# Kernel optimization log

Hardware: AMD Instinct MI355X
Metric: run time of the kernel (lower is better)

Reference implementation:

```python
import jax, jax.numpy as jnp
import numpy as np

D = 1024  # d = D_in // 3
GAMMA = 5.0
EPS_NORM = 1e-5
EPS_W = 1e-8


def batch_affine_norm(x, g, b):
    # normalize over batch+time dims, per-feature affine
    mean = x.mean(axis=(0, 1))
    var = x.var(axis=(0, 1))
    return (x - mean) / jnp.sqrt(var + EPS_NORM) * g + b


def block(xi, w, b, a, g, beta):
    # xi: (B,T,d) -> (B,T,d,3)
    # PositiveLinearHK(1->3): softplus-positive weight + bias, per channel
    h = xi[..., None] * jax.nn.softplus(w) + b          # (B,T,d,3)
    # SingleStiefelProjector(3): orthogonalize learned 3x3 via QR, apply
    Q, _ = jnp.linalg.qr(a)                             # (d,3,3)
    h = jnp.einsum('btdi,dij->btdj', h, Q)
    return batch_affine_norm(h, g, beta)


def setup_inputs() -> dict:
    key = jax.random.key(0)
    ks = jax.random.split(key, 20)
    B, T = 4, 2048
    inp = {'x': jax.random.normal(ks[0], (B, T, 3 * D), dtype=jnp.float32)}
    i = 1
    for p in ('q', 'k', 'v'):
        inp['w' + p] = jax.random.normal(ks[i], (D, 3), dtype=jnp.float32) * 0.5; i += 1
        inp['b' + p] = jnp.zeros((D, 3), dtype=jnp.float32)
        inp['a' + p] = jax.random.normal(ks[i], (D, 3, 3), dtype=jnp.float32); i += 1
        inp['g' + p] = jnp.ones((D, 3), dtype=jnp.float32)
        inp['beta' + p] = jnp.zeros((D, 3), dtype=jnp.float32)
    inp['g_out'] = jnp.ones((D,), dtype=jnp.float32)
    inp['b_out'] = jnp.zeros((D,), dtype=jnp.float32)
    return inp


def reference(x, wq, bq, aq, gq, betaq, wk, bk, ak, gk, betak, wv, bv, av, gv, betav, g_out, b_out):
    d = D
    Qp = block(x[..., :d], wq, bq, aq, gq, betaq)        # (B,T,d,3)
    Kp = block(x[..., d:2 * d], wk, bk, ak, gk, betak)
    Vp = block(x[..., 2 * d:], wv, bv, av, gv, betav)
    scores = jax.nn.sigmoid(GAMMA * (Qp * Kp))
    weights = scores / (scores.sum(axis=-1, keepdims=True) + EPS_W)
    out = (weights * Vp).sum(axis=-1)                    # (B,T,d)
    return batch_affine_norm(out, g_out, b_out)
```

## Files before the change

### kernel.cpp

```cpp
#include <hip/hip_runtime.h>
#include <math.h>

namespace {

constexpr int DD = 1024;
constexpr int NC = 3072;
constexpr int NG = 768;
constexpr int DG = 256;
constexpr int NROWS = 8192;
constexpr int CH1 = 64;
constexpr int CH2 = 256;
constexpr float GAMMA = 5.0f;
constexpr float EPS_NORM = 1e-5f;
constexpr float EPS_W = 1e-8f;
constexpr float ZCLAMP = 15.0f;

struct Params {
  const float *x;
  const float *wq, *aq, *gq, *betaq;
  const float *wk, *ak, *gk, *betak;
  const float *wv, *av, *gv, *betav;
  const float *g_out, *b_out;
  float *out;
  float *psum, *psq;
  float *A_arr, *B_arr;
  float *opsum, *opsq;
  float *om, *osc, *ob;
  float *o_arr;
};

__device__ __forceinline__ void acc4(float4& s, float4& q, float4 v) {
  s.x += v.x; s.y += v.y; s.z += v.z; s.w += v.w;
  q.x += v.x * v.x; q.y += v.y * v.y; q.z += v.z * v.z; q.w += v.w * v.w;
}
__device__ __forceinline__ void add4(float4& s, float4 v) {
  s.x += v.x; s.y += v.y; s.z += v.z; s.w += v.w;
}

__device__ __forceinline__ void qr_coef(const Params& P, int c, float mean, float var) {
  int p = c >> 10;
  int d = c & (DD - 1);
  const float* w    = (p == 0) ? P.wq    : (p == 1) ? P.wk    : P.wv;
  const float* a    = (p == 0) ? P.aq    : (p == 1) ? P.ak    : P.av;
  const float* g    = (p == 0) ? P.gq    : (p == 1) ? P.gk    : P.gv;
  const float* beta = (p == 0) ? P.betaq : (p == 1) ? P.betak : P.betav;
  float gam = (p == 0) ? GAMMA : 1.0f;

  float A[3][3];
  #pragma unroll
  for (int i = 0; i < 3; ++i)
    #pragma unroll
    for (int j = 0; j < 3; ++j) A[i][j] = a[(d * 3 + i) * 3 + j];

  float v1y = 0.f, v1z = 0.f, v2z = 0.f, t1 = 0.f, t2 = 0.f;
  {
    float alpha = A[0][0];
    float xn2 = A[1][0] * A[1][0] + A[2][0] * A[2][0];
    if (xn2 > 0.f) {
      float beta_ = -copysignf(sqrtf(alpha * alpha + xn2), alpha);
      t1 = (beta_ - alpha) / beta_;
      float inv = 1.0f / (alpha - beta_);
      v1y = A[1][0] * inv; v1z = A[2][0] * inv;
      #pragma unroll
      for (int j = 1; j < 3; ++j) {
        float dot = A[0][j] + A[1][j] * v1y + A[2][j] * v1z;
        float f = t1 * dot;
        A[0][j] -= f; A[1][j] -= f * v1y; A[2][j] -= f * v1z;
      }
    }
  }
  {
    float alpha = A[1][1], x2 = A[2][1];
    if (x2 != 0.f) {
      float beta_ = -copysignf(sqrtf(alpha * alpha + x2 * x2), alpha);
      t2 = (beta_ - alpha) / beta_;
      v2z = x2 / (alpha - beta_);
    }
  }
  float v1[3] = {1.f, v1y, v1z};
  float v2[3] = {0.f, 1.f, v2z};
  float v12 = v1y + v1z * v2z;
  float sp0 = log1pf(expf(w[d * 3 + 0]));
  float sp1 = log1pf(expf(w[d * 3 + 1]));
  float sp2 = log1pf(expf(w[d * 3 + 2]));
  #pragma unroll
  for (int j = 0; j < 3; ++j) {
    float Q0 = ((0 == j) ? 1.f : 0.f) - t1 * v1[0] * v1[j] - t2 * v2[0] * v2[j]
               + t1 * t2 * v12 * v1[0] * v2[j];
    float Q1 = ((1 == j) ? 1.f : 0.f) - t1 * v1[1] * v1[j] - t2 * v2[1] * v2[j]
               + t1 * t2 * v12 * v1[1] * v2[j];
    float Q2 = ((2 == j) ? 1.f : 0.f) - t1 * v1[2] * v1[j] - t2 * v2[2] * v2[j]
               + t1 * t2 * v12 * v1[2] * v2[j];
    float W = sp0 * Q0 + sp1 * Q1 + sp2 * Q2;
    float s = W * g[d * 3 + j] / sqrtf(W * W * var + EPS_NORM);
    P.A_arr[j * NC + c] = gam * s;
    P.B_arr[j * NC + c] = gam * (beta[d * 3 + j] - mean * s);
  }
}

struct CoefReg {
  float4 Aq[3], Bq[3], Ak[3], Bk[3], Av[3], Bv[3];
};

__device__ __forceinline__ CoefReg load_coefs(const Params& P, int tg) {
  CoefReg C;
  #pragma unroll
  for (int j = 0; j < 3; ++j) {
    C.Aq[j] = ((const float4*)(P.A_arr + j * NC))[tg];
    C.Ak[j] = ((const float4*)(P.A_arr + j * NC + DD))[tg];
    C.Av[j] = ((const float4*)(P.A_arr + j * NC + 2 * DD))[tg];
    C.Bq[j] = ((const float4*)(P.B_arr + j * NC))[tg];
    C.Bk[j] = ((const float4*)(P.B_arr + j * NC + DD))[tg];
    C.Bv[j] = ((const float4*)(P.B_arr + j * NC + 2 * DD))[tg];
  }
  return C;
}

__device__ __forceinline__ float4 contract4(float4 xq, float4 xk, float4 xv,
                                            const CoefReg& C) {
  float4 ov;
  #pragma unroll
  for (int kk = 0; kk < 4; ++kk) {
    float xqv = ((const float*)&xq)[kk];
    float xkv = ((const float*)&xk)[kk];
    float xvv = ((const float*)&xv)[kk];
    float Q[3], K[3], V[3];
    #pragma unroll
    for (int j = 0; j < 3; ++j) {
      Q[j] = fmaf(xqv, ((const float*)&C.Aq[j])[kk], ((const float*)&C.Bq[j])[kk]);
      K[j] = fmaf(xkv, ((const float*)&C.Ak[j])[kk], ((const float*)&C.Bk[j])[kk]);
      V[j] = fmaf(xvv, ((const float*)&C.Av[j])[kk], ((const float*)&C.Bv[j])[kk]);
    }
    float e0 = __expf(fminf(Q[0] * K[0], ZCLAMP));
    float e1 = __expf(fminf(Q[1] * K[1], ZCLAMP));
    float e2 = __expf(fminf(Q[2] * K[2], ZCLAMP));
    float a0 = 1.f + e0, a1 = 1.f + e1, a2 = 1.f + e2;
    float a01 = a0 * a1, a12 = a1 * a2, a02 = a0 * a2;
    float w0 = e0 * a12, w1 = e1 * a02, w2 = e2 * a01;
    float num = w0 * V[0] + w1 * V[1] + w2 * V[2];
    float den = w0 + w1 + w2 + EPS_W * (a01 * a2);
    ((float*)&ov)[kk] = num / den;
  }
  return ov;
}

__global__ __launch_bounds__(256, 4) void k1_col_stats(Params P) {
  __shared__ float4 lds_s[4][64];
  __shared__ float4 lds_q[4][64];
  const int t = threadIdx.x;
  const int lane = t & 63;
  const int slice = t >> 6;
  const int cg = blockIdx.x * 64 + lane;
  const int r0 = blockIdx.y * 128 + slice * 32;
  const float4* x4 = (const float4*)P.x;
  float4 s = {0,0,0,0}, q = {0,0,0,0};
  #pragma unroll 8
  for (int r = 0; r < 32; ++r) {
    acc4(s, q, x4[(size_t)(r0 + r) * NG + cg]);
  }
  lds_s[slice][lane] = s;
  lds_q[slice][lane] = q;
  __syncthreads();
  if (t < 64) {
    float4 ss = lds_s[0][t], qq = lds_q[0][t];
    #pragma unroll
    for (int i = 1; i < 4; ++i) { add4(ss, lds_s[i][t]); add4(qq, lds_q[i][t]); }
    ((float4*)(P.psum + (size_t)blockIdx.y * NC))[blockIdx.x * 64 + t] = ss;
    ((float4*)(P.psq + (size_t)blockIdx.y * NC))[blockIdx.x * 64 + t] = qq;
  }
}

__global__ __launch_bounds__(256, 4) void k2_coef(Params P) {
  __shared__ float lds_s[4][64];
  __shared__ float lds_q[4][64];
  const int t = threadIdx.x;
  const int lane = t & 63;
  const int slice = t >> 6;
  const int c = blockIdx.x * 64 + lane;
  float s = 0.f, q = 0.f;
  #pragma unroll
  for (int i = 0; i < 16; ++i) {
    int ch = slice * 16 + i;
    s += P.psum[(size_t)ch * NC + c];
    q += P.psq[(size_t)ch * NC + c];
  }
  lds_s[slice][lane] = s;
  lds_q[slice][lane] = q;
  __syncthreads();
  if (t < 64) {
    float ss = lds_s[0][t] + lds_s[1][t] + lds_s[2][t] + lds_s[3][t];
    float qq = lds_q[0][t] + lds_q[1][t] + lds_q[2][t] + lds_q[3][t];
    float mean = ss / NROWS;
    float var = qq / NROWS - mean * mean;
    if (var < 0.f) var = 0.f;
    qr_coef(P, blockIdx.x * 64 + t, mean, var);
  }
}

__global__ __launch_bounds__(256, 3) void k3_main(Params P) {
  __shared__ float4 lds_s[4][64];
  __shared__ float4 lds_q[4][64];
  const int t = threadIdx.x;
  const int lane = t & 63;
  const int slice = t >> 6;
  const int tg = blockIdx.x * 64 + lane;
  const int r0 = blockIdx.y * 32 + slice * 8;
  const float4* x4 = (const float4*)P.x;
  float4* o4 = (float4*)P.o_arr;
  CoefReg C = load_coefs(P, tg);
  float4 s = {0,0,0,0}, q = {0,0,0,0};
  #pragma unroll
  for (int r = 0; r < 8; ++r) {
    size_t base = (size_t)(r0 + r) * NG;
    float4 xq = x4[base + tg];
    float4 xk = x4[base + 256 + tg];
    float4 xv = x4[base + 512 + tg];
    float4 ov = contract4(xq, xk, xv, C);
    o4[(size_t)(r0 + r) * DG + tg] = ov;
    acc4(s, q, ov);
  }
  lds_s[slice][lane] = s;
  lds_q[slice][lane] = q;
  __syncthreads();
  if (t < 64) {
    float4 ss = lds_s[0][t], qq = lds_q[0][t];
    #pragma unroll
    for (int i = 1; i < 4; ++i) { add4(ss, lds_s[i][t]); add4(qq, lds_q[i][t]); }
    ((float4*)(P.opsum + (size_t)blockIdx.y * DD))[blockIdx.x * 64 + t] = ss;
    ((float4*)(P.opsq + (size_t)blockIdx.y * DD))[blockIdx.x * 64 + t] = qq;
  }
}

__global__ __launch_bounds__(256, 4) void k4_out_stats(Params P) {
  __shared__ float lds_s[4][64];
  __shared__ float lds_q[4][64];
  const int t = threadIdx.x;
  const int lane = t & 63;
  const int slice = t >> 6;
  const int d = blockIdx.x * 64 + lane;
  float s = 0.f, q = 0.f;
  #pragma unroll 8
  for (int i = 0; i < 64; ++i) {
    int ch = slice * 64 + i;
    s += P.opsum[(size_t)ch * DD + d];
    q += P.opsq[(size_t)ch * DD + d];
  }
  lds_s[slice][lane] = s;
  lds_q[slice][lane] = q;
  __syncthreads();
  if (t < 64) {
    int dd = blockIdx.x * 64 + t;
    float ss = lds_s[0][t] + lds_s[1][t] + lds_s[2][t] + lds_s[3][t];
    float qq = lds_q[0][t] + lds_q[1][t] + lds_q[2][t] + lds_q[3][t];
    float mean = ss / NROWS;
    float var = qq / NROWS - mean * mean;
    if (var < 0.f) var = 0.f;
    P.om[dd] = mean;
    P.osc[dd] = P.g_out[dd] / sqrtf(var + EPS_NORM);
    P.ob[dd] = P.b_out[dd];
  }
}

__global__ __launch_bounds__(256, 8) void k5_final(Params P) {
  const int t = threadIdx.x;
  const int r0 = blockIdx.x * 4;
  float4 m = ((const float4*)P.om)[t];
  float4 sc = ((const float4*)P.osc)[t];
  float4 bb = ((const float4*)P.ob)[t];
  const float4* o4 = (const float4*)P.o_arr;
  float4* out4 = (float4*)P.out;
  #pragma unroll
  for (int rr = 0; rr < 4; ++rr) {
    size_t idx = (size_t)(r0 + rr) * DG + t;
    float4 o = o4[idx];
    float4 y;
    y.x = (o.x - m.x) * sc.x + bb.x;
    y.y = (o.y - m.y) * sc.y + bb.y;
    y.z = (o.z - m.z) * sc.z + bb.z;
    y.w = (o.w - m.w) * sc.w + bb.w;
    out4[idx] = y;
  }
}

}

extern "C" void kernel_launch(void* const* d_in, const int* in_sizes, int n_in,
                              void* d_out, int out_size, void* d_ws, size_t ws_size,
                              hipStream_t stream) {
  Params P;
  P.x     = (const float*)d_in[0];
  P.wq    = (const float*)d_in[1];
  P.aq    = (const float*)d_in[3];
  P.gq    = (const float*)d_in[4];
  P.betaq = (const float*)d_in[5];
  P.wk    = (const float*)d_in[6];
  P.ak    = (const float*)d_in[8];
  P.gk    = (const float*)d_in[9];
  P.betak = (const float*)d_in[10];
  P.wv    = (const float*)d_in[11];
  P.av    = (const float*)d_in[13];
  P.gv    = (const float*)d_in[14];
  P.betav = (const float*)d_in[15];
  P.g_out = (const float*)d_in[16];
  P.b_out = (const float*)d_in[17];
  P.out   = (float*)d_out;

  float* ws = (float*)d_ws;
  P.psum  = ws;  ws += (size_t)CH1 * NC;
  P.psq   = ws;  ws += (size_t)CH1 * NC;
  P.A_arr = ws;  ws += 3 * NC;
  P.B_arr = ws;  ws += 3 * NC;
  P.opsum = ws;  ws += (size_t)CH2 * DD;
  P.opsq  = ws;  ws += (size_t)CH2 * DD;
  P.om    = ws;  ws += DD;
  P.osc   = ws;  ws += DD;
  P.ob    = ws;  ws += DD;
  P.o_arr = ws;  ws += (size_t)NROWS * DD;

  k1_col_stats<<<dim3(12, 64), dim3(256), 0, stream>>>(P);
  k2_coef<<<dim3(48), dim3(256), 0, stream>>>(P);
  k3_main<<<dim3(4, 256), dim3(256), 0, stream>>>(P);
  k4_out_stats<<<dim3(16), dim3(256), 0, stream>>>(P);
  k5_final<<<dim3(2048), dim3(256), 0, stream>>>(P);
}
```

Baseline: 66.25 us.

## Replace partial-sum buffers with atomic column reductions and fuse output stats into final kernel

```diff
diff --git a/kernel.cpp b/kernel.cpp
--- a/kernel.cpp
+++ b/kernel.cpp
@@ -8,12 +8,12 @@
 constexpr int NG = 768;
 constexpr int DG = 256;
 constexpr int NROWS = 8192;
-constexpr int CH1 = 64;
-constexpr int CH2 = 256;
 constexpr float GAMMA = 5.0f;
 constexpr float EPS_NORM = 1e-5f;
 constexpr float EPS_W = 1e-8f;
 constexpr float ZCLAMP = 15.0f;
+
+typedef float nfloat4 __attribute__((ext_vector_type(4)));
 
 struct Params {
   const float *x;
@@ -22,19 +22,15 @@
   const float *wv, *av, *gv, *betav;
   const float *g_out, *b_out;
   float *out;
-  float *psum, *psq;
+  float *colsum, *colsq;
   float *A_arr, *B_arr;
-  float *opsum, *opsq;
-  float *om, *osc, *ob;
+  float *osum, *osq;
   float *o_arr;
 };
 
 __device__ __forceinline__ void acc4(float4& s, float4& q, float4 v) {
   s.x += v.x; s.y += v.y; s.z += v.z; s.w += v.w;
   q.x += v.x * v.x; q.y += v.y * v.y; q.z += v.z * v.z; q.w += v.w * v.w;
-}
-__device__ __forceinline__ void add4(float4& s, float4 v) {
-  s.x += v.x; s.y += v.y; s.z += v.z; s.w += v.w;
 }
 
 __device__ __forceinline__ void qr_coef(const Params& P, int c, float mean, float var) {
@@ -161,40 +157,24 @@
   lds_s[slice][lane] = s;
   lds_q[slice][lane] = q;
   __syncthreads();
-  if (t < 64) {
-    float4 ss = lds_s[0][t], qq = lds_q[0][t];
-    #pragma unroll
-    for (int i = 1; i < 4; ++i) { add4(ss, lds_s[i][t]); add4(qq, lds_q[i][t]); }
-    ((float4*)(P.psum + (size_t)blockIdx.y * NC))[blockIdx.x * 64 + t] = ss;
-    ((float4*)(P.psq + (size_t)blockIdx.y * NC))[blockIdx.x * 64 + t] = qq;
-  }
+  float ssum = 0.f, ssq = 0.f;
+  #pragma unroll
+  for (int i = 0; i < 4; ++i) {
+    ssum += ((const float*)&lds_s[i][t >> 2])[t & 3];
+    ssq  += ((const float*)&lds_q[i][t >> 2])[t & 3];
+  }
+  atomicAdd(&P.colsum[blockIdx.x * 256 + t], ssum);
+  atomicAdd(&P.colsq[blockIdx.x * 256 + t], ssq);
 }
 
 __global__ __launch_bounds__(256, 4) void k2_coef(Params P) {
-  __shared__ float lds_s[4][64];
-  __shared__ float lds_q[4][64];
-  const int t = threadIdx.x;
-  const int lane = t & 63;
-  const int slice = t >> 6;
-  const int c = blockIdx.x * 64 + lane;
-  float s = 0.f, q = 0.f;
-  #pragma unroll
-  for (int i = 0; i < 16; ++i) {
-    int ch = slice * 16 + i;
-    s += P.psum[(size_t)ch * NC + c];
-    q += P.psq[(size_t)ch * NC + c];
-  }
-  lds_s[slice][lane] = s;
-  lds_q[slice][lane] = q;
-  __syncthreads();
-  if (t < 64) {
-    float ss = lds_s[0][t] + lds_s[1][t] + lds_s[2][t] + lds_s[3][t];
-    float qq = lds_q[0][t] + lds_q[1][t] + lds_q[2][t] + lds_q[3][t];
-    float mean = ss / NROWS;
-    float var = qq / NROWS - mean * mean;
-    if (var < 0.f) var = 0.f;
-    qr_coef(P, blockIdx.x * 64 + t, mean, var);
-  }
+  const int c = blockIdx.x * 256 + threadIdx.x;
+  float s = P.colsum[c];
+  float q = P.colsq[c];
+  float mean = s / NROWS;
+  float var = q / NROWS - mean * mean;
+  if (var < 0.f) var = 0.f;
+  qr_coef(P, c, mean, var);
 }
 
 __global__ __launch_bounds__(256, 3) void k3_main(Params P) {
@@ -222,63 +202,44 @@
   lds_s[slice][lane] = s;
   lds_q[slice][lane] = q;
   __syncthreads();
-  if (t < 64) {
-    float4 ss = lds_s[0][t], qq = lds_q[0][t];
-    #pragma unroll
-    for (int i = 1; i < 4; ++i) { add4(ss, lds_s[i][t]); add4(qq, lds_q[i][t]); }
-    ((float4*)(P.opsum + (size_t)blockIdx.y * DD))[blockIdx.x * 64 + t] = ss;
-    ((float4*)(P.opsq + (size_t)blockIdx.y * DD))[blockIdx.x * 64 + t] = qq;
-  }
-}
-
-__global__ __launch_bounds__(256, 4) void k4_out_stats(Params P) {
-  __shared__ float lds_s[4][64];
-  __shared__ float lds_q[4][64];
+  float ssum = 0.f, ssq = 0.f;
+  #pragma unroll
+  for (int i = 0; i < 4; ++i) {
+    ssum += ((const float*)&lds_s[i][t >> 2])[t & 3];
+    ssq  += ((const float*)&lds_q[i][t >> 2])[t & 3];
+  }
+  atomicAdd(&P.osum[blockIdx.x * 256 + t], ssum);
+  atomicAdd(&P.osq[blockIdx.x * 256 + t], ssq);
+}
+
+__global__ __launch_bounds__(256, 8) void k4_final(Params P) {
   const int t = threadIdx.x;
-  const int lane = t & 63;
-  const int slice = t >> 6;
-  const int d = blockIdx.x * 64 + lane;
-  float s = 0.f, q = 0.f;
-  #pragma unroll 8
-  for (int i = 0; i < 64; ++i) {
-    int ch = slice * 64 + i;
-    s += P.opsum[(size_t)ch * DD + d];
-    q += P.opsq[(size_t)ch * DD + d];
-  }
-  lds_s[slice][lane] = s;
-  lds_q[slice][lane] = q;
-  __syncthreads();
-  if (t < 64) {
-    int dd = blockIdx.x * 64 + t;
-    float ss = lds_s[0][t] + lds_s[1][t] + lds_s[2][t] + lds_s[3][t];
-    float qq = lds_q[0][t] + lds_q[1][t] + lds_q[2][t] + lds_q[3][t];
-    float mean = ss / NROWS;
-    float var = qq / NROWS - mean * mean;
+  float4 s4 = ((const float4*)P.osum)[t];
+  float4 q4 = ((const float4*)P.osq)[t];
+  float4 g4 = ((const float4*)P.g_out)[t];
+  float4 b4 = ((const float4*)P.b_out)[t];
+  float4 m, sc;
+  #pragma unroll
+  for (int kk = 0; kk < 4; ++kk) {
+    float mean = ((const float*)&s4)[kk] / NROWS;
+    float var = ((const float*)&q4)[kk] / NROWS - mean * mean;
     if (var < 0.f) var = 0.f;
-    P.om[dd] = mean;
-    P.osc[dd] = P.g_out[dd] / sqrtf(var + EPS_NORM);
-    P.ob[dd] = P.b_out[dd];
-  }
-}
-
-__global__ __launch_bounds__(256, 8) void k5_final(Params P) {
-  const int t = threadIdx.x;
+    ((float*)&m)[kk] = mean;
+    ((float*)&sc)[kk] = ((const float*)&g4)[kk] / sqrtf(var + EPS_NORM);
+  }
   const int r0 = blockIdx.x * 4;
-  float4 m = ((const float4*)P.om)[t];
-  float4 sc = ((const float4*)P.osc)[t];
-  float4 bb = ((const float4*)P.ob)[t];
   const float4* o4 = (const float4*)P.o_arr;
   float4* out4 = (float4*)P.out;
   #pragma unroll
   for (int rr = 0; rr < 4; ++rr) {
     size_t idx = (size_t)(r0 + rr) * DG + t;
     float4 o = o4[idx];
-    float4 y;
-    y.x = (o.x - m.x) * sc.x + bb.x;
-    y.y = (o.y - m.y) * sc.y + bb.y;
-    y.z = (o.z - m.z) * sc.z + bb.z;
-    y.w = (o.w - m.w) * sc.w + bb.w;
-    out4[idx] = y;
+    nfloat4 y;
+    y.x = (o.x - m.x) * sc.x + b4.x;
+    y.y = (o.y - m.y) * sc.y + b4.y;
+    y.z = (o.z - m.z) * sc.z + b4.z;
+    y.w = (o.w - m.w) * sc.w + b4.w;
+    __builtin_nontemporal_store(y, (nfloat4*)&out4[idx]);
   }
 }
 
@@ -306,20 +267,17 @@
   P.out   = (float*)d_out;
 
   float* ws = (float*)d_ws;
-  P.psum  = ws;  ws += (size_t)CH1 * NC;
-  P.psq   = ws;  ws += (size_t)CH1 * NC;
-  P.A_arr = ws;  ws += 3 * NC;
-  P.B_arr = ws;  ws += 3 * NC;
-  P.opsum = ws;  ws += (size_t)CH2 * DD;
-  P.opsq  = ws;  ws += (size_t)CH2 * DD;
-  P.om    = ws;  ws += DD;
-  P.osc   = ws;  ws += DD;
-  P.ob    = ws;  ws += DD;
-  P.o_arr = ws;  ws += (size_t)NROWS * DD;
-
+  P.colsum = ws;  ws += NC;
+  P.colsq  = ws;  ws += NC;
+  P.osum   = ws;  ws += DD;
+  P.osq    = ws;  ws += DD;
+  P.A_arr  = ws;  ws += 3 * NC;
+  P.B_arr  = ws;  ws += 3 * NC;
+  P.o_arr  = ws;  ws += (size_t)NROWS * DD;
+
+  (void)hipMemsetAsync(P.colsum, 0, (2 * NC + 2 * DD) * sizeof(float), stream);
   k1_col_stats<<<dim3(12, 64), dim3(256), 0, stream>>>(P);
-  k2_coef<<<dim3(48), dim3(256), 0, stream>>>(P);
+  k2_coef<<<dim3(12), dim3(256), 0, stream>>>(P);
   k3_main<<<dim3(4, 256), dim3(256), 0, stream>>>(P);
-  k4_out_stats<<<dim3(16), dim3(256), 0, stream>>>(P);
-  k5_final<<<dim3(2048), dim3(256), 0, stream>>>(P);
-}
+  k4_final<<<dim3(2048), dim3(256), 0, stream>>>(P);
+}
```

New measurement: 64.20 us. 1.03x faster.
